# Optimization experiments

Measured on AMD Instinct MI355X. Metric: run time of the kernel, lower is better.

The kernel has to match this reference:

```python
import jax, jax.numpy as jnp
import numpy as np

N, E, IN, HID = 8192, 8192, 256, 256
DEG_P = 0.004  # avg degree ~32


def setup_inputs() -> dict:
    key = jax.random.key(0)
    ks = jax.random.split(key, 16)
    x = jax.random.normal(ks[0], (N, IN), dtype=jnp.float32)
    adj = (jax.random.uniform(ks[1], (N, N)) < DEG_P).astype(jnp.float32)
    tar_ei = jax.random.randint(ks[2], (2, E), 0, N, dtype=jnp.int32)
    s = 0.05
    return {
        'x': x, 'adj': adj, 'tar_ei': tar_ei,
        'W1c': jax.random.normal(ks[3], (IN, HID)) * s, 'b1c': jnp.zeros((HID,)),
        'W2c': jax.random.normal(ks[4], (HID, HID)) * s, 'b2c': jnp.zeros((HID,)),
        'W1j': jax.random.normal(ks[5], (IN, HID)) * s, 'b1j': jnp.zeros((HID,)),
        'W2j': jax.random.normal(ks[6], (HID, HID)) * s, 'b2j': jnp.zeros((HID,)),
        'Wl1': jax.random.normal(ks[7], (HID, HID)) * s, 'bl1': jnp.zeros((HID,)),
        'Wl2': jax.random.normal(ks[8], (HID, HID)) * s, 'bl2': jnp.zeros((HID,)),
        'Wout': jax.random.normal(ks[9], (HID, 1)) * s, 'bout': jnp.zeros((1,)),
    }


def _mlp2(h, W1, b1, W2, b2):
    # Linear -> ReLU -> (Dropout: eval-mode identity) -> Linear
    return jax.nn.relu(h @ W1 + b1) @ W2 + b2


def reference(x, adj, tar_ei, W1c, b1c, W2c, b2c, W1j, b1j, W2j, b2j,
              Wl1, bl1, Wl2, bl2, Wout, bout):
    beta = 1.0
    xi = x[tar_ei[0]]            # [E, IN]
    xj = x[tar_ei[1]]            # [E, IN]
    ai = adj[tar_ei[0]]          # [E, N] gathered adjacency rows
    aj = adj[tar_ei[1]]          # [E, N]
    # common-neighbor overlap + spmm_add aggregation: cn = ai*aj; xcn = cn @ x
    xcn = (ai * aj) @ x          # [E, IN]
    xij = _mlp2(xi * xj, W1j, b1j, W2j, b2j)
    xcn = _mlp2(xcn, W1c, b1c, W2c, b2c)
    h = beta * xcn + xij
    h = jax.nn.relu(h @ Wl1 + bl1)
    h = jax.nn.relu(h @ Wl2 + bl2)
    out = h @ Wout + bout        # [E, 1]
    return out.squeeze()
```

## Files before the change

kernel.cpp:

```cpp
#include <hip/hip_runtime.h>
#include <stdint.h>

#define NN 8192
#define NE 8192
#define DIM 256
#define NW 128
#define HCAP 64
#define TE 32

typedef short bf16x8 __attribute__((ext_vector_type(8)));
typedef float f32x4 __attribute__((ext_vector_type(4)));

__device__ __forceinline__ unsigned short f2bf(float f) {
  uint32_t u = __builtin_bit_cast(uint32_t, f);
  u += 0x7fffu + ((u >> 16) & 1u);
  return (unsigned short)(u >> 16);
}
__device__ __forceinline__ float bf2f(unsigned short h) {
  uint32_t u = ((uint32_t)h) << 16;
  return __builtin_bit_cast(float, u);
}

__global__ __launch_bounds__(256) void prep_kernel(
    const float* __restrict__ adj,
    const float* __restrict__ W1c, const float* __restrict__ W2c,
    const float* __restrict__ W1j, const float* __restrict__ W2j,
    const float* __restrict__ Wl1, const float* __restrict__ Wl2,
    unsigned short* __restrict__ Wt,
    unsigned long long* __restrict__ bits) {
  const int blk = blockIdx.x;
  if (blk < 4096) {
    const float4* __restrict__ adjv = (const float4*)adj;
    const int lane = threadIdx.x & 63;
    const int wv = blk * 4 + (threadIdx.x >> 6);
    const int nwv = 4096 * 4;
    const int total = NN * 32;
    for (int t = 4 * wv; t < total; t += 4 * nwv) {
      float4 v0 = adjv[(size_t)((t + 0) >> 5) * 2048 + ((t + 0) & 31) * 64 + lane];
      float4 v1 = adjv[(size_t)((t + 1) >> 5) * 2048 + ((t + 1) & 31) * 64 + lane];
      float4 v2 = adjv[(size_t)((t + 2) >> 5) * 2048 + ((t + 2) & 31) * 64 + lane];
      float4 v3 = adjv[(size_t)((t + 3) >> 5) * 2048 + ((t + 3) & 31) * 64 + lane];
      unsigned long long m00 = __ballot(v0.x != 0.0f);
      unsigned long long m01 = __ballot(v0.y != 0.0f);
      unsigned long long m02 = __ballot(v0.z != 0.0f);
      unsigned long long m03 = __ballot(v0.w != 0.0f);
      unsigned long long m10 = __ballot(v1.x != 0.0f);
      unsigned long long m11 = __ballot(v1.y != 0.0f);
      unsigned long long m12 = __ballot(v1.z != 0.0f);
      unsigned long long m13 = __ballot(v1.w != 0.0f);
      unsigned long long m20 = __ballot(v2.x != 0.0f);
      unsigned long long m21 = __ballot(v2.y != 0.0f);
      unsigned long long m22 = __ballot(v2.z != 0.0f);
      unsigned long long m23 = __ballot(v2.w != 0.0f);
      unsigned long long m30 = __ballot(v3.x != 0.0f);
      unsigned long long m31 = __ballot(v3.y != 0.0f);
      unsigned long long m32 = __ballot(v3.z != 0.0f);
      unsigned long long m33 = __ballot(v3.w != 0.0f);
      if (lane == 0) {
        unsigned long long* p = bits + (size_t)(t >> 5) * NW + (t & 31) * 4;
        p[0]  = m00; p[1]  = m01; p[2]  = m02; p[3]  = m03;
        p[4]  = m10; p[5]  = m11; p[6]  = m12; p[7]  = m13;
        p[8]  = m20; p[9]  = m21; p[10] = m22; p[11] = m23;
        p[12] = m30; p[13] = m31; p[14] = m32; p[15] = m33;
      }
    }
  } else {
    const float* Ws[6] = {W1c, W2c, W1j, W2j, Wl1, Wl2};
    const int b = blk - 4096;
    const int w = b >> 8;
    const int n = b & 255;
    const int k = threadIdx.x;
    Wt[w * 65536 + n * DIM + k] = f2bf(Ws[w][k * DIM + n]);
  }
}


#define LDP 264

__device__ __forceinline__ void load_w16(const unsigned short* __restrict__ Wt,
                                         bf16x8 w[8], int lane, int wave) {
  const int lr = lane & 15;
  const int kl = (lane >> 4) * 8;
  const int n0 = wave * 16;
#pragma unroll
  for (int kk = 0; kk < 8; ++kk)
    w[kk] = *(const bf16x8*)(Wt + (size_t)(n0 + lr) * DIM + kk * 32 + kl);
}

__device__ __forceinline__ void gemm16(const unsigned short (*src)[LDP],
                                       const bf16x8 w[8],
                                       f32x4 acc[2], int lane) {
  const int lr = lane & 15;
  const int kl = (lane >> 4) * 8;
#pragma unroll
  for (int kk = 0; kk < 8; ++kk) {
    const int k0 = kk * 32 + kl;
    bf16x8 a0 = *(const bf16x8*)(&src[lr][k0]);
    bf16x8 a1 = *(const bf16x8*)(&src[16 + lr][k0]);
    acc[0] = __builtin_amdgcn_mfma_f32_16x16x32_bf16(a0, w[kk], acc[0], 0, 0, 0);
    acc[1] = __builtin_amdgcn_mfma_f32_16x16x32_bf16(a1, w[kk], acc[1], 0, 0, 0);
  }
}

__device__ __forceinline__ void epilogue16(f32x4 acc[2], float bb, bool relu,
                                           unsigned short (*dst)[LDP],
                                           int lane, int wave) {
  const int lc = lane & 15;
  const int rg = (lane >> 4) * 4;
  const int col = wave * 16 + lc;
#pragma unroll
  for (int m = 0; m < 2; ++m)
#pragma unroll
    for (int q = 0; q < 4; ++q) {
      float v = acc[m][q] + bb;
      if (relu) v = fmaxf(v, 0.f);
      dst[m * 16 + rg + q][col] = f2bf(v);
    }
}

__global__ __launch_bounds__(1024) void fused_kernel(
    const float* __restrict__ x,
    const unsigned long long* __restrict__ bits,
    const int* __restrict__ tar,
    const unsigned short* __restrict__ Wt,
    const float* __restrict__ b1c, const float* __restrict__ b2c,
    const float* __restrict__ b1j, const float* __restrict__ b2j,
    const float* __restrict__ bl1, const float* __restrict__ bl2,
    const float* __restrict__ Wout, const float* __restrict__ bout,
    float* __restrict__ out) {
  __shared__ unsigned short lA[TE][LDP];
  __shared__ unsigned short lB[TE][LDP];
  __shared__ unsigned short lC[TE][LDP];
  __shared__ int hits[TE][HCAP];
  __shared__ int nh[TE];

  const int tid = threadIdx.x;
  const int lane = tid & 63;
  const int wave = tid >> 6;
  const int e0 = blockIdx.x * TE;

  const int lc = lane & 15;
  const int c0 = wave * 16 + lc;
  const float vb1c = b1c[c0];
  const float vb1j = b1j[c0];
  const float vb2 = b2c[c0] + b2j[c0];
  const float vbl1 = bl1[c0];
  const float vbl2 = bl2[c0];
  const int gpart = tid & 31;
  float wv[8];
#pragma unroll
  for (int q = 0; q < 8; ++q) wv[q] = Wout[gpart * 8 + q];
  const float vbout = bout[0];

  if (tid < TE) nh[tid] = 0;

  const int e_a = tid >> 5;
  const int t32 = tid & 31;
  const int ia = tar[e0 + e_a];
  const int ja = tar[NE + e0 + e_a];
  unsigned long long bw_i[4], bw_j[4];
  {
    const unsigned long long* bi = bits + (size_t)ia * NW + t32 * 4;
    const unsigned long long* bj = bits + (size_t)ja * NW + t32 * 4;
#pragma unroll
    for (int q = 0; q < 4; ++q) { bw_i[q] = bi[q]; bw_j[q] = bj[q]; }
  }

  {
    const int col = tid & 255;
    const int sub = tid >> 8;
    float vi[8], vj[8];
#pragma unroll
    for (int p = 0; p < 8; ++p) {
      const int e = sub * 8 + p;
      vi[p] = x[(size_t)tar[e0 + e] * DIM + col];
      vj[p] = x[(size_t)tar[NE + e0 + e] * DIM + col];
    }
#pragma unroll
    for (int p = 0; p < 8; ++p)
      lC[sub * 8 + p][col] = f2bf(vi[p] * vj[p]);
  }
  __syncthreads();

#pragma unroll
  for (int q = 0; q < 4; ++q) {
    unsigned long long m = bw_i[q] & bw_j[q];
    const int base = t32 << 8;
    while (m) {
      int b = __builtin_ctzll(m);
      m &= m - 1;
      int idx = atomicAdd(&nh[e_a], 1);
      if (idx < HCAP) hits[e_a][idx] = base + (b << 2) + q;
    }
  }
  __syncthreads();

  bf16x8 wX[8], wY[8];
  load_w16(Wt + 0 * 65536, wX, lane, wave);
  load_w16(Wt + 1 * 65536, wY, lane, wave);
  {
    const int col = tid & 255;
    const int sub = tid >> 8;
#pragma unroll
    for (int p = 0; p < 8; ++p) {
      const int e = sub * 8 + p;
      const int n = nh[e] < HCAP ? nh[e] : HCAP;
      float xc = 0.f;
      for (int h = 0; h < n; ++h)
        xc += x[(size_t)hits[e][h] * DIM + col];
      lA[e][col] = f2bf(xc);
    }
  }
  __syncthreads();

  f32x4 acc[2], pAcc[2];
  const f32x4 z4 = {0.f, 0.f, 0.f, 0.f};

  acc[0] = z4; acc[1] = z4;
  gemm16(lA, wX, acc, lane);
  load_w16(Wt + 2 * 65536, wX, lane, wave);
  epilogue16(acc, vb1c, true, lB, lane, wave);
  __syncthreads();

  pAcc[0] = z4; pAcc[1] = z4;
  gemm16(lB, wY, pAcc, lane);
  load_w16(Wt + 3 * 65536, wY, lane, wave);
  acc[0] = z4; acc[1] = z4;
  gemm16(lC, wX, acc, lane);
  epilogue16(acc, vb1j, true, lA, lane, wave);
  __syncthreads();

  gemm16(lA, wY, pAcc, lane);
  load_w16(Wt + 4 * 65536, wX, lane, wave);
  {
    const int rg = (lane >> 4) * 4;
    const int col = wave * 16 + lc;
#pragma unroll
    for (int m = 0; m < 2; ++m)
#pragma unroll
      for (int q = 0; q < 4; ++q)
        lB[m * 16 + rg + q][col] = f2bf(pAcc[m][q] + vb2);
  }
  __syncthreads();

  acc[0] = z4; acc[1] = z4;
  gemm16(lB, wX, acc, lane);
  load_w16(Wt + 5 * 65536, wY, lane, wave);
  epilogue16(acc, vbl1, true, lA, lane, wave);
  __syncthreads();

  acc[0] = z4; acc[1] = z4;
  gemm16(lA, wY, acc, lane);
  epilogue16(acc, vbl2, true, lB, lane, wave);
  __syncthreads();

  const int el = tid >> 5;
  float s = 0.f;
#pragma unroll
  for (int q = 0; q < 8; ++q)
    s += bf2f(lB[el][gpart * 8 + q]) * wv[q];
#pragma unroll
  for (int o = 16; o; o >>= 1) s += __shfl_xor(s, o);
  if (gpart == 0) out[e0 + el] = s + vbout;
}

extern "C" void kernel_launch(void* const* d_in, const int* in_sizes, int n_in,
                              void* d_out, int out_size, void* d_ws, size_t ws_size,
                              hipStream_t stream) {
  const float* x    = (const float*)d_in[0];
  const float* adj  = (const float*)d_in[1];
  const int*   tar  = (const int*)d_in[2];
  const float* W1c  = (const float*)d_in[3];
  const float* b1c  = (const float*)d_in[4];
  const float* W2c  = (const float*)d_in[5];
  const float* b2c  = (const float*)d_in[6];
  const float* W1j  = (const float*)d_in[7];
  const float* b1j  = (const float*)d_in[8];
  const float* W2j  = (const float*)d_in[9];
  const float* b2j  = (const float*)d_in[10];
  const float* Wl1  = (const float*)d_in[11];
  const float* bl1  = (const float*)d_in[12];
  const float* Wl2  = (const float*)d_in[13];
  const float* bl2  = (const float*)d_in[14];
  const float* Wout = (const float*)d_in[15];
  const float* bout = (const float*)d_in[16];

  char* ws = (char*)d_ws;
  unsigned short*     Wt   = (unsigned short*)(ws);
  unsigned long long* bits = (unsigned long long*)(ws + (1u << 20));

  prep_kernel<<<4096 + 1536, 256, 0, stream>>>(adj, W1c, W2c, W1j, W2j, Wl1,
                                               Wl2, Wt, bits);

  fused_kernel<<<NE / TE, 1024, 0, stream>>>(x, bits, tar, Wt, b1c, b2c, b1j,
                                             b2j, bl1, bl2, Wout, bout,
                                             (float*)d_out);
}
```

Before: 78.96 us.

## Double edge tile to 64 per block and restructure MLP GEMM chain

Raises the per-block edge tile from 32 to 64, so each wave issues four MFMA row tiles per weight fragment and each weight load from global memory serves twice as many edges. The GEMM sequence is reordered to use a single accumulator set, with the combined second-layer output staged in LDS, and the Wout reduction now uses float4 loads over 16 lanes. It also moves the weight-transpose blocks ahead of the adjacency bitmask blocks in the prep kernel. The block grid halves to 128 blocks, which leaves fewer blocks than the device has compute units, and LDS usage per block doubles.

```diff
diff --git a/kernel.cpp b/kernel.cpp
--- a/kernel.cpp
+++ b/kernel.cpp
@@ -6,7 +6,7 @@
 #define DIM 256
 #define NW 128
 #define HCAP 64
-#define TE 32
+#define TE 64
 
 typedef short bf16x8 __attribute__((ext_vector_type(8)));
 typedef float f32x4 __attribute__((ext_vector_type(4)));
@@ -29,10 +29,16 @@
     unsigned short* __restrict__ Wt,
     unsigned long long* __restrict__ bits) {
   const int blk = blockIdx.x;
-  if (blk < 4096) {
+  if (blk < 1536) {
+    const float* Ws[6] = {W1c, W2c, W1j, W2j, Wl1, Wl2};
+    const int w = blk >> 8;
+    const int n = blk & 255;
+    const int k = threadIdx.x;
+    Wt[w * 65536 + n * DIM + k] = f2bf(Ws[w][k * DIM + n]);
+  } else {
     const float4* __restrict__ adjv = (const float4*)adj;
     const int lane = threadIdx.x & 63;
-    const int wv = blk * 4 + (threadIdx.x >> 6);
+    const int wv = (blk - 1536) * 4 + (threadIdx.x >> 6);
     const int nwv = 4096 * 4;
     const int total = NN * 32;
     for (int t = 4 * wv; t < total; t += 4 * nwv) {
@@ -64,13 +70,6 @@
         p[12] = m30; p[13] = m31; p[14] = m32; p[15] = m33;
       }
     }
-  } else {
-    const float* Ws[6] = {W1c, W2c, W1j, W2j, Wl1, Wl2};
-    const int b = blk - 4096;
-    const int w = b >> 8;
-    const int n = b & 255;
-    const int k = threadIdx.x;
-    Wt[w * 65536 + n * DIM + k] = f2bf(Ws[w][k * DIM + n]);
   }
 }
 
@@ -87,9 +86,9 @@
     w[kk] = *(const bf16x8*)(Wt + (size_t)(n0 + lr) * DIM + kk * 32 + kl);
 }
 
-__device__ __forceinline__ void gemm16(const unsigned short (*src)[LDP],
+__device__ __forceinline__ void gemm64(const unsigned short (*src)[LDP],
                                        const bf16x8 w[8],
-                                       f32x4 acc[2], int lane) {
+                                       f32x4 acc[4], int lane) {
   const int lr = lane & 15;
   const int kl = (lane >> 4) * 8;
 #pragma unroll
@@ -97,19 +96,28 @@
     const int k0 = kk * 32 + kl;
     bf16x8 a0 = *(const bf16x8*)(&src[lr][k0]);
     bf16x8 a1 = *(const bf16x8*)(&src[16 + lr][k0]);
+    bf16x8 a2 = *(const bf16x8*)(&src[32 + lr][k0]);
+    bf16x8 a3 = *(const bf16x8*)(&src[48 + lr][k0]);
     acc[0] = __builtin_amdgcn_mfma_f32_16x16x32_bf16(a0, w[kk], acc[0], 0, 0, 0);
     acc[1] = __builtin_amdgcn_mfma_f32_16x16x32_bf16(a1, w[kk], acc[1], 0, 0, 0);
-  }
-}
-
-__device__ __forceinline__ void epilogue16(f32x4 acc[2], float bb, bool relu,
+    acc[2] = __builtin_amdgcn_mfma_f32_16x16x32_bf16(a2, w[kk], acc[2], 0, 0, 0);
+    acc[3] = __builtin_amdgcn_mfma_f32_16x16x32_bf16(a3, w[kk], acc[3], 0, 0, 0);
+  }
+}
+
+__device__ __forceinline__ void zero4(f32x4 a[4]) {
+  const f32x4 z = {0.f, 0.f, 0.f, 0.f};
+  a[0] = z; a[1] = z; a[2] = z; a[3] = z;
+}
+
+__device__ __forceinline__ void epilogue64(f32x4 acc[4], float bb, bool relu,
                                            unsigned short (*dst)[LDP],
                                            int lane, int wave) {
   const int lc = lane & 15;
   const int rg = (lane >> 4) * 4;
   const int col = wave * 16 + lc;
 #pragma unroll
-  for (int m = 0; m < 2; ++m)
+  for (int m = 0; m < 4; ++m)
 #pragma unroll
     for (int q = 0; q < 4; ++q) {
       float v = acc[m][q] + bb;
@@ -146,51 +154,48 @@
   const float vb2 = b2c[c0] + b2j[c0];
   const float vbl1 = bl1[c0];
   const float vbl2 = bl2[c0];
-  const int gpart = tid & 31;
-  float wv[8];
-#pragma unroll
-  for (int q = 0; q < 8; ++q) wv[q] = Wout[gpart * 8 + q];
-  const float vbout = bout[0];
 
   if (tid < TE) nh[tid] = 0;
 
-  const int e_a = tid >> 5;
-  const int t32 = tid & 31;
-  const int ia = tar[e0 + e_a];
-  const int ja = tar[NE + e0 + e_a];
-  unsigned long long bw_i[4], bw_j[4];
+  const int e_a = tid >> 4;
+  const int t16 = tid & 15;
+  unsigned long long bw_i[8], bw_j[8];
   {
-    const unsigned long long* bi = bits + (size_t)ia * NW + t32 * 4;
-    const unsigned long long* bj = bits + (size_t)ja * NW + t32 * 4;
-#pragma unroll
-    for (int q = 0; q < 4; ++q) { bw_i[q] = bi[q]; bw_j[q] = bj[q]; }
+    const int ia = tar[e0 + e_a];
+    const int ja = tar[NE + e0 + e_a];
+    const unsigned long long* bi = bits + (size_t)ia * NW + t16 * 8;
+    const unsigned long long* bj = bits + (size_t)ja * NW + t16 * 8;
+#pragma unroll
+    for (int q = 0; q < 8; ++q) { bw_i[q] = bi[q]; bw_j[q] = bj[q]; }
   }
 
   {
     const int col = tid & 255;
     const int sub = tid >> 8;
-    float vi[8], vj[8];
-#pragma unroll
-    for (int p = 0; p < 8; ++p) {
-      const int e = sub * 8 + p;
+    float vi[16], vj[16];
+#pragma unroll
+    for (int p = 0; p < 16; ++p) {
+      const int e = sub * 16 + p;
       vi[p] = x[(size_t)tar[e0 + e] * DIM + col];
       vj[p] = x[(size_t)tar[NE + e0 + e] * DIM + col];
     }
 #pragma unroll
-    for (int p = 0; p < 8; ++p)
-      lC[sub * 8 + p][col] = f2bf(vi[p] * vj[p]);
-  }
-  __syncthreads();
-
-#pragma unroll
-  for (int q = 0; q < 4; ++q) {
+    for (int p = 0; p < 16; ++p)
+      lC[sub * 16 + p][col] = f2bf(vi[p] * vj[p]);
+  }
+  __syncthreads();
+
+#pragma unroll
+  for (int q = 0; q < 8; ++q) {
     unsigned long long m = bw_i[q] & bw_j[q];
-    const int base = t32 << 8;
+    const int w = t16 * 8 + q;
+    const int base = (w >> 2) << 8;
+    const int qq = w & 3;
     while (m) {
       int b = __builtin_ctzll(m);
       m &= m - 1;
       int idx = atomicAdd(&nh[e_a], 1);
-      if (idx < HCAP) hits[e_a][idx] = base + (b << 2) + q;
+      if (idx < HCAP) hits[e_a][idx] = base + (b << 2) + qq;
     }
   }
   __syncthreads();
@@ -202,8 +207,8 @@
     const int col = tid & 255;
     const int sub = tid >> 8;
 #pragma unroll
-    for (int p = 0; p < 8; ++p) {
-      const int e = sub * 8 + p;
+    for (int p = 0; p < 16; ++p) {
+      const int e = sub * 16 + p;
       const int n = nh[e] < HCAP ? nh[e] : HCAP;
       float xc = 0.f;
       for (int h = 0; h < n; ++h)
@@ -213,55 +218,54 @@
   }
   __syncthreads();
 
-  f32x4 acc[2], pAcc[2];
-  const f32x4 z4 = {0.f, 0.f, 0.f, 0.f};
-
-  acc[0] = z4; acc[1] = z4;
-  gemm16(lA, wX, acc, lane);
+  f32x4 acc[4];
+
+  zero4(acc);
+  gemm64(lA, wX, acc, lane);
   load_w16(Wt + 2 * 65536, wX, lane, wave);
-  epilogue16(acc, vb1c, true, lB, lane, wave);
-  __syncthreads();
-
-  pAcc[0] = z4; pAcc[1] = z4;
-  gemm16(lB, wY, pAcc, lane);
-  load_w16(Wt + 3 * 65536, wY, lane, wave);
-  acc[0] = z4; acc[1] = z4;
-  gemm16(lC, wX, acc, lane);
-  epilogue16(acc, vb1j, true, lA, lane, wave);
-  __syncthreads();
-
-  gemm16(lA, wY, pAcc, lane);
-  load_w16(Wt + 4 * 65536, wX, lane, wave);
+  epilogue64(acc, vb1c, true, lB, lane, wave);
+  __syncthreads();
+
+  zero4(acc);
+  gemm64(lC, wX, acc, lane);
+  load_w16(Wt + 3 * 65536, wX, lane, wave);
+  epilogue64(acc, vb1j, true, lA, lane, wave);
+  __syncthreads();
+
+  zero4(acc);
+  gemm64(lB, wY, acc, lane);
+  gemm64(lA, wX, acc, lane);
+  load_w16(Wt + 4 * 65536, wY, lane, wave);
+  load_w16(Wt + 5 * 65536, wX, lane, wave);
+  epilogue64(acc, vb2, false, lC, lane, wave);
+  __syncthreads();
+
+  zero4(acc);
+  gemm64(lC, wY, acc, lane);
+  epilogue64(acc, vbl1, true, lA, lane, wave);
+  __syncthreads();
+
+  zero4(acc);
+  gemm64(lA, wX, acc, lane);
+  epilogue64(acc, vbl2, true, lB, lane, wave);
+  __syncthreads();
+
   {
-    const int rg = (lane >> 4) * 4;
-    const int col = wave * 16 + lc;
-#pragma unroll
-    for (int m = 0; m < 2; ++m)
-#pragma unroll
-      for (int q = 0; q < 4; ++q)
-        lB[m * 16 + rg + q][col] = f2bf(pAcc[m][q] + vb2);
-  }
-  __syncthreads();
-
-  acc[0] = z4; acc[1] = z4;
-  gemm16(lB, wX, acc, lane);
-  load_w16(Wt + 5 * 65536, wY, lane, wave);
-  epilogue16(acc, vbl1, true, lA, lane, wave);
-  __syncthreads();
-
-  acc[0] = z4; acc[1] = z4;
-  gemm16(lA, wY, acc, lane);
-  epilogue16(acc, vbl2, true, lB, lane, wave);
-  __syncthreads();
-
-  const int el = tid >> 5;
-  float s = 0.f;
-#pragma unroll
-  for (int q = 0; q < 8; ++q)
-    s += bf2f(lB[el][gpart * 8 + q]) * wv[q];
-#pragma unroll
-  for (int o = 16; o; o >>= 1) s += __shfl_xor(s, o);
-  if (gpart == 0) out[e0 + el] = s + vbout;
+    const int el = tid >> 4;
+    const int gp = tid & 15;
+    const float4* __restrict__ w4 = (const float4*)Wout;
+    float s = 0.f;
+#pragma unroll
+    for (int q4 = 0; q4 < 4; ++q4) {
+      const float4 wq = w4[gp * 4 + q4];
+      const int c = gp * 16 + q4 * 4;
+      s += bf2f(lB[el][c + 0]) * wq.x + bf2f(lB[el][c + 1]) * wq.y +
+           bf2f(lB[el][c + 2]) * wq.z + bf2f(lB[el][c + 3]) * wq.w;
+    }
+#pragma unroll
+    for (int o = 8; o; o >>= 1) s += __shfl_xor(s, o);
+    if (gp == 0) out[e0 + el] = s + bout[0];
+  }
 }
 
 extern "C" void kernel_launch(void* const* d_in, const int* in_sizes, int n_in,
@@ -289,7 +293,7 @@
   unsigned short*     Wt   = (unsigned short*)(ws);
   unsigned long long* bits = (unsigned long long*)(ws + (1u << 20));
 
-  prep_kernel<<<4096 + 1536, 256, 0, stream>>>(adj, W1c, W2c, W1j, W2j, Wl1,
+  prep_kernel<<<1536 + 4096, 256, 0, stream>>>(adj, W1c, W2c, W1j, W2j, Wl1,
                                                Wl2, Wt, bits);
 
   fused_kernel<<<NE / TE, 1024, 0, stream>>>(x, bits, tar, Wt, b1c, b2c, b1j,
```

Result: slower. 86.68 us (+9.8%).

## Reorder MLP stages to overlap gather with GEMM and fuse final projection

Applied to the files above, without the earlier changes.

Moves the weight-transpose blocks ahead of the adjacency bitmask blocks in the prep kernel. In the fused kernel, the xij branch GEMM now runs while the common-neighbor gather sums are held in registers. The two second-layer GEMMs accumulate into one accumulator, which drops one barrier stage. The last layer's ReLU and the Wout dot product run in registers with shuffles and a small shared reduction, instead of writing bf16 to LDS and reading it back. This removes a sync and an LDS round trip and hides gather latency, at the cost of more live registers in a 1024-thread block.

```diff
diff --git a/kernel.cpp b/kernel.cpp
--- a/kernel.cpp
+++ b/kernel.cpp
@@ -29,10 +29,16 @@
     unsigned short* __restrict__ Wt,
     unsigned long long* __restrict__ bits) {
   const int blk = blockIdx.x;
-  if (blk < 4096) {
+  if (blk < 1536) {
+    const float* Ws[6] = {W1c, W2c, W1j, W2j, Wl1, Wl2};
+    const int w = blk >> 8;
+    const int n = blk & 255;
+    const int k = threadIdx.x;
+    Wt[w * 65536 + n * DIM + k] = f2bf(Ws[w][k * DIM + n]);
+  } else {
     const float4* __restrict__ adjv = (const float4*)adj;
     const int lane = threadIdx.x & 63;
-    const int wv = blk * 4 + (threadIdx.x >> 6);
+    const int wv = (blk - 1536) * 4 + (threadIdx.x >> 6);
     const int nwv = 4096 * 4;
     const int total = NN * 32;
     for (int t = 4 * wv; t < total; t += 4 * nwv) {
@@ -64,13 +70,6 @@
         p[12] = m30; p[13] = m31; p[14] = m32; p[15] = m33;
       }
     }
-  } else {
-    const float* Ws[6] = {W1c, W2c, W1j, W2j, Wl1, Wl2};
-    const int b = blk - 4096;
-    const int w = b >> 8;
-    const int n = b & 255;
-    const int k = threadIdx.x;
-    Wt[w * 65536 + n * DIM + k] = f2bf(Ws[w][k * DIM + n]);
   }
 }
 
@@ -133,6 +132,7 @@
   __shared__ unsigned short lC[TE][LDP];
   __shared__ int hits[TE][HCAP];
   __shared__ int nh[TE];
+  __shared__ float sPart[16][TE];
 
   const int tid = threadIdx.x;
   const int lane = tid & 63;
@@ -146,20 +146,17 @@
   const float vb2 = b2c[c0] + b2j[c0];
   const float vbl1 = bl1[c0];
   const float vbl2 = bl2[c0];
-  const int gpart = tid & 31;
-  float wv[8];
-#pragma unroll
-  for (int q = 0; q < 8; ++q) wv[q] = Wout[gpart * 8 + q];
+  const float vwout = Wout[c0];
   const float vbout = bout[0];
 
   if (tid < TE) nh[tid] = 0;
 
   const int e_a = tid >> 5;
   const int t32 = tid & 31;
-  const int ia = tar[e0 + e_a];
-  const int ja = tar[NE + e0 + e_a];
   unsigned long long bw_i[4], bw_j[4];
   {
+    const int ia = tar[e0 + e_a];
+    const int ja = tar[NE + e0 + e_a];
     const unsigned long long* bi = bits + (size_t)ia * NW + t32 * 4;
     const unsigned long long* bj = bits + (size_t)ja * NW + t32 * 4;
 #pragma unroll
@@ -180,6 +177,9 @@
     for (int p = 0; p < 8; ++p)
       lC[sub * 8 + p][col] = f2bf(vi[p] * vj[p]);
   }
+  bf16x8 wX[8], wY[8];
+  load_w16(Wt + 2 * 65536, wX, lane, wave);
+  load_w16(Wt + 0 * 65536, wY, lane, wave);
   __syncthreads();
 
 #pragma unroll
@@ -195,73 +195,86 @@
   }
   __syncthreads();
 
-  bf16x8 wX[8], wY[8];
-  load_w16(Wt + 0 * 65536, wX, lane, wave);
-  load_w16(Wt + 1 * 65536, wY, lane, wave);
+  f32x4 acc[2];
+  const f32x4 z4 = {0.f, 0.f, 0.f, 0.f};
+
   {
     const int col = tid & 255;
     const int sub = tid >> 8;
+    float xc[8];
 #pragma unroll
     for (int p = 0; p < 8; ++p) {
       const int e = sub * 8 + p;
       const int n = nh[e] < HCAP ? nh[e] : HCAP;
-      float xc = 0.f;
+      float s = 0.f;
       for (int h = 0; h < n; ++h)
-        xc += x[(size_t)hits[e][h] * DIM + col];
-      lA[e][col] = f2bf(xc);
-    }
-  }
-  __syncthreads();
-
-  f32x4 acc[2], pAcc[2];
-  const f32x4 z4 = {0.f, 0.f, 0.f, 0.f};
+        s += x[(size_t)hits[e][h] * DIM + col];
+      xc[p] = s;
+    }
+    acc[0] = z4; acc[1] = z4;
+    gemm16(lC, wX, acc, lane);
+    load_w16(Wt + 1 * 65536, wX, lane, wave);
+    epilogue16(acc, vb1j, true, lB, lane, wave);
+#pragma unroll
+    for (int p = 0; p < 8; ++p)
+      lA[sub * 8 + p][col] = f2bf(xc[p]);
+  }
+  __syncthreads();
+
+  acc[0] = z4; acc[1] = z4;
+  gemm16(lA, wY, acc, lane);
+  load_w16(Wt + 3 * 65536, wY, lane, wave);
+  epilogue16(acc, vb1c, true, lC, lane, wave);
+  __syncthreads();
+
+  acc[0] = z4; acc[1] = z4;
+  gemm16(lC, wX, acc, lane);
+  gemm16(lB, wY, acc, lane);
+  load_w16(Wt + 4 * 65536, wX, lane, wave);
+  load_w16(Wt + 5 * 65536, wY, lane, wave);
+  epilogue16(acc, vb2, false, lA, lane, wave);
+  __syncthreads();
 
   acc[0] = z4; acc[1] = z4;
   gemm16(lA, wX, acc, lane);
-  load_w16(Wt + 2 * 65536, wX, lane, wave);
-  epilogue16(acc, vb1c, true, lB, lane, wave);
-  __syncthreads();
-
-  pAcc[0] = z4; pAcc[1] = z4;
-  gemm16(lB, wY, pAcc, lane);
-  load_w16(Wt + 3 * 65536, wY, lane, wave);
+  epilogue16(acc, vbl1, true, lB, lane, wave);
+  __syncthreads();
+
   acc[0] = z4; acc[1] = z4;
-  gemm16(lC, wX, acc, lane);
-  epilogue16(acc, vb1j, true, lA, lane, wave);
-  __syncthreads();
-
-  gemm16(lA, wY, pAcc, lane);
-  load_w16(Wt + 4 * 65536, wX, lane, wave);
+  gemm16(lB, wY, acc, lane);
   {
     const int rg = (lane >> 4) * 4;
-    const int col = wave * 16 + lc;
+    float v[2][4];
 #pragma unroll
     for (int m = 0; m < 2; ++m)
 #pragma unroll
-      for (int q = 0; q < 4; ++q)
-        lB[m * 16 + rg + q][col] = f2bf(pAcc[m][q] + vb2);
-  }
-  __syncthreads();
-
-  acc[0] = z4; acc[1] = z4;
-  gemm16(lB, wX, acc, lane);
-  load_w16(Wt + 5 * 65536, wY, lane, wave);
-  epilogue16(acc, vbl1, true, lA, lane, wave);
-  __syncthreads();
-
-  acc[0] = z4; acc[1] = z4;
-  gemm16(lA, wY, acc, lane);
-  epilogue16(acc, vbl2, true, lB, lane, wave);
-  __syncthreads();
-
-  const int el = tid >> 5;
-  float s = 0.f;
-#pragma unroll
-  for (int q = 0; q < 8; ++q)
-    s += bf2f(lB[el][gpart * 8 + q]) * wv[q];
-#pragma unroll
-  for (int o = 16; o; o >>= 1) s += __shfl_xor(s, o);
-  if (gpart == 0) out[e0 + el] = s + vbout;
+      for (int q = 0; q < 4; ++q) {
+        float h3 = fmaxf(acc[m][q] + vbl2, 0.f);
+        v[m][q] = h3 * vwout;
+      }
+#pragma unroll
+    for (int o = 1; o < 16; o <<= 1)
+#pragma unroll
+      for (int m = 0; m < 2; ++m)
+#pragma unroll
+        for (int q = 0; q < 4; ++q)
+          v[m][q] += __shfl_xor(v[m][q], o);
+    if (lc == 0) {
+#pragma unroll
+      for (int m = 0; m < 2; ++m)
+#pragma unroll
+        for (int q = 0; q < 4; ++q)
+          sPart[wave][m * 16 + rg + q] = v[m][q];
+    }
+  }
+  __syncthreads();
+
+  if (tid < TE) {
+    float s = 0.f;
+#pragma unroll
+    for (int w = 0; w < 16; ++w) s += sPart[w][tid];
+    out[e0 + tid] = s + vbout;
+  }
 }
 
 extern "C" void kernel_launch(void* const* d_in, const int* in_sizes, int n_in,
@@ -289,7 +302,7 @@
   unsigned short*     Wt   = (unsigned short*)(ws);
   unsigned long long* bits = (unsigned long long*)(ws + (1u << 20));
 
-  prep_kernel<<<4096 + 1536, 256, 0, stream>>>(adj, W1c, W2c, W1j, W2j, Wl1,
+  prep_kernel<<<1536 + 4096, 256, 0, stream>>>(adj, W1c, W2c, W1j, W2j, Wl1,
                                                Wl2, Wt, bits);
 
   fused_kernel<<<NE / TE, 1024, 0, stream>>>(x, bits, tar, Wt, b1c, b2c, b1j,
```

New measurement: 79.75 us. Within noise of the previous version (+1.0%).
